# Performance work log

Hardware: AMD Instinct MI355X
Metric: run time of the kernel (lower is better)

Reference implementation:

```python
import jax, jax.numpy as jnp
import numpy as np
from jax import lax

B, T = 64, 256
N_INPUT, H, R, N_OUT, F = 161, 1024, 1024, 161, 64
KF, KT = 21, 11  # context
CONV_H = (N_INPUT - KF) // 2 + 1  # 71
RNN_IN = F * CONV_H  # 4544


def setup_inputs() -> dict:
    key = jax.random.key(0)
    ks = iter(jax.random.split(key, 40))
    s = 0.05
    rn = lambda shape, scale=s: jax.random.normal(next(ks), shape, jnp.float32) * scale
    inp = {
        'x': rn((B, 1, N_INPUT, T), 1.0),
        'h1': jnp.zeros((B, H), jnp.float32),
        'h2': jnp.zeros((B, H), jnp.float32),
        'h3': jnp.zeros((B, H), jnp.float32),
        # conv input layer
        'conv_W': rn((F, 1, KF, KT)),
        'conv_b': jnp.zeros((F,), jnp.float32),
        # GRU cells (bias=False), torch gate order [r, z, n]
        'W_ih0': rn((3 * H, RNN_IN)), 'W_hh0': rn((3 * H, H)),
        'W_ih1': rn((3 * H, H)),      'W_hh1': rn((3 * H, H)),
        'W_ih2': rn((3 * H, H)),      'W_hh2': rn((3 * H, H)),
        # in_transitions (n_input -> H)
        'in1_W': rn((H, N_INPUT)), 'in1_b': jnp.zeros((H,), jnp.float32),
        'in2_W': rn((H, N_INPUT)), 'in2_b': jnp.zeros((H,), jnp.float32),
        # h_transitions (H -> H)
        'ht0_W': rn((H, H)), 'ht0_b': jnp.zeros((H,), jnp.float32),
        'ht1_W': rn((H, H)), 'ht1_b': jnp.zeros((H,), jnp.float32),
        'ht2_W': rn((H, H)), 'ht2_b': jnp.zeros((H,), jnp.float32),
        # out_transitions (H -> R)
        'ot0_W': rn((R, H)), 'ot0_b': jnp.zeros((R,), jnp.float32),
        'ot1_W': rn((R, H)), 'ot1_b': jnp.zeros((R,), jnp.float32),
        'ot2_W': rn((R, H)), 'ot2_b': jnp.zeros((R,), jnp.float32),
        # output layer (R -> n_output), init uniform(-0.1, 0.1), bias 0
        'out_W': jax.random.uniform(next(ks), (N_OUT, R), jnp.float32, -0.1, 0.1),
        'out_b': jnp.zeros((N_OUT,), jnp.float32),
    }
    return inp


def _gru(x_gates, h, W_hh):
    # x_gates: (B, 3H) = x @ W_ih.T ; torch GRUCell, no bias
    hg = h @ W_hh.T
    xr, xz, xn = jnp.split(x_gates, 3, axis=-1)
    hr, hz, hn = jnp.split(hg, 3, axis=-1)
    r = jax.nn.sigmoid(xr + hr)
    z = jax.nn.sigmoid(xz + hz)
    n = jnp.tanh(xn + r * hn)
    return (1.0 - z) * n + z * h


def reference(x, h1, h2, h3, conv_W, conv_b,
              W_ih0, W_hh0, W_ih1, W_hh1, W_ih2, W_hh2,
              in1_W, in1_b, in2_W, in2_b,
              ht0_W, ht0_b, ht1_W, ht1_b, ht2_W, ht2_b,
              ot0_W, ot0_b, ot1_W, ot1_b, ot2_W, ot2_b,
              out_W, out_b):
    pad_t = (KT - 1) // 2
    # Conv2d(1, F, (21,11), stride=(2,1), padding=(0,5)) -> (B, F, CONV_H, T)
    y_conv = lax.conv_general_dilated(
        x, conv_W, window_strides=(2, 1), padding=((0, 0), (pad_t, pad_t)),
        dimension_numbers=('NCHW', 'OIHW', 'NCHW')) + conv_b[None, :, None, None]
    b, t = x.shape[0], x.shape[3]
    x_rnn = y_conv.reshape(b, RNN_IN, t).transpose(2, 0, 1)  # (T, B, RNN_IN)
    x0 = x[:, 0, :, :].transpose(2, 0, 1)                    # (T, B, N_INPUT)
    # Precompute all time-parallel input projections (big GEMMs outside scan)
    xg0 = jnp.einsum('tbi,gi->tbg', x_rnn, W_ih0)            # (T, B, 3H)
    x2_all = x0 @ in1_W.T + in1_b                            # (T, B, H)
    x3_all = x0 @ in2_W.T + in2_b                            # (T, B, H)

    def step(carry, inp):
        h1, h2, h3 = carry
        xg0_t, x2_t, x3_t = inp
        h1 = _gru(xg0_t, h1, W_hh0)
        h1_to_h2 = h1 @ ht0_W.T + ht0_b
        h1_to_h3 = h1 @ ht1_W.T + ht1_b
        r1 = h1 @ ot0_W.T + ot0_b
        h2 = _gru((x2_t + h1_to_h2) @ W_ih1.T, h2, W_hh1)
        h2_to_h3 = h1_to_h2 @ ht2_W.T + ht2_b  # note: applied to h1_to_h2, as in source
        r2 = h2 @ ot1_W.T + ot1_b
        h3 = _gru((x3_t + h1_to_h3 + h2_to_h3) @ W_ih2.T, h3, W_hh2)
        r3 = h3 @ ot2_W.T + ot2_b
        y_t = (r1 + r2 + r3) @ out_W.T + out_b
        return (h1, h2, h3), y_t

    _, y = lax.scan(step, (h1, h2, h3), (xg0, x2_all, x3_all))
    return y  # (T, B, N_OUT)
```

## Files before the change

### kernel.cpp

```cpp
#include <hip/hip_runtime.h>
#include <hip/hip_cooperative_groups.h>
#include <stdint.h>

namespace cg = cooperative_groups;

typedef __bf16 bf16x8 __attribute__((ext_vector_type(8)));
typedef float f32x4 __attribute__((ext_vector_type(4)));

#define MFMA16(a,b,c) __builtin_amdgcn_mfma_f32_16x16x32_bf16((a),(b),(c),0,0,0)

__device__ __forceinline__ float bf2f(unsigned short u){
  union { float f; unsigned int i; } v; v.i = ((unsigned int)u)<<16; return v.f;
}
__device__ __forceinline__ unsigned short f2bf(float f){
  union { float f; unsigned int i; } v; v.f = f;
  unsigned int r = v.i + 0x7FFFu + ((v.i>>16)&1u);
  return (unsigned short)(r>>16);
}
__device__ __forceinline__ bf16x8 ldg8(const unsigned short* p){ return *(const bf16x8*)p; }
__device__ __forceinline__ bf16x8 lds8(const short* p){ return *(const bf16x8*)p; }
__device__ __forceinline__ float sigm(float x){ return 1.f/(1.f+__expf(-x)); }
__device__ __forceinline__ float tanhc(float x){
  x = fminf(fmaxf(x,-30.f),30.f);
  float e = __expf(2.f*x);
  return (e-1.f)/(e+1.f);
}

__device__ __forceinline__ void wait_ge(unsigned int* c, int need){
  if (need <= 0) return;
  int guard = 0;
  while ((int)__hip_atomic_load(c, __ATOMIC_RELAXED, __HIP_MEMORY_SCOPE_AGENT) < need){
    __builtin_amdgcn_s_sleep(8);
    if (++guard > 4000000) break;
  }
}


__global__ void k_f2b(unsigned short* __restrict__ dst, const float* __restrict__ src, int n){
  int i = blockIdx.x*256 + threadIdx.x;
  if (i < n) dst[i] = f2bf(src[i]);
}

__global__ void k_zero(unsigned int* __restrict__ p, int nwords){
  int i = blockIdx.x*256 + threadIdx.x;
  if (i < nwords) p[i] = 0u;
}

__global__ void k_transpose(unsigned short* __restrict__ dst, const float* __restrict__ src,
                            int DR, int DC, int srcRowLen){
  __shared__ float tile[32][33];
  int r0 = blockIdx.x*32, c0 = blockIdx.y*32;
  int tx = threadIdx.x, ty = threadIdx.y;
  #pragma unroll
  for (int i=0;i<4;i++){
    int c = c0 + ty + i*8, r = r0 + tx;
    float v = 0.f;
    if (c < DC && r < srcRowLen) v = src[(size_t)c*srcRowLen + r];
    tile[ty+i*8][tx] = v;
  }
  __syncthreads();
  #pragma unroll
  for (int i=0;i<4;i++){
    int r = r0 + ty + i*8, c = c0 + tx;
    if (r < DR && c < DC) dst[(size_t)r*DC + c] = f2bf(tile[tx][ty+i*8]);
  }
}

__global__ void k_im2col(unsigned short* __restrict__ Xcol, const float* __restrict__ x, int t0){
  long long idx = (long long)blockIdx.x*256 + threadIdx.x;
  if (idx >= (long long)8192*1792) return;
  int row = (int)(idx / 1792), c = (int)(idx % 1792);
  int t = t0 + (row >> 6), b = row & 63;
  float v = 0.f;
  if (c < 1771){
    int kt = c / 161, i = c % 161;
    int tt = t + kt - 5;
    if (tt >= 0 && tt < 256) v = x[((size_t)b*161 + i)*256 + tt];
  }
  Xcol[idx] = f2bf(v);
}

__global__ void k_x0p(unsigned short* __restrict__ x0p, const float* __restrict__ x){
  int idx = blockIdx.x*256 + threadIdx.x;
  if (idx >= 16384*192) return;
  int row = idx / 192, i = idx % 192;
  int t = row >> 6, b = row & 63;
  float v = 0.f;
  if (i < 161) v = x[((size_t)b*161 + i)*256 + t];
  x0p[idx] = f2bf(v);
}

__global__ void k_cmatT(unsigned short* __restrict__ dst, const float* __restrict__ convW){
  int idx = blockIdx.x*256 + threadIdx.x;
  if (idx >= 1792*4544) return;
  int crow = idx / 4544, col = idx % 4544;
  float v = 0.f;
  if (crow < 1771){
    int kt = crow / 161, i = crow % 161;
    int f = col / 71, ch = col % 71;
    int kf = i - 2*ch;
    if (kf >= 0 && kf < 21) v = convW[((size_t)f*21 + kf)*11 + kt];
  }
  dst[idx] = f2bf(v);
}

__global__ void k_cbexp(float* __restrict__ dst, const float* __restrict__ convb){
  int i = blockIdx.x*256 + threadIdx.x;
  if (i < 4544) dst[i] = convb[i/71];
}

__global__ void k_add4(float* __restrict__ dst, const float* a, const float* b,
                       const float* c, const float* d, int n){
  int i = blockIdx.x*256 + threadIdx.x;
  if (i >= n) return;
  float v = a ? a[i] : 0.f;
  if (b) v += b[i];
  if (c) v += c[i];
  if (d) v += d[i];
  dst[i] = v;
}

__global__ void k_matvec(float* __restrict__ out, const float* __restrict__ A, int lda, int K,
                         const float* __restrict__ v, const float* __restrict__ addv, int M){
  int row = blockIdx.x*4 + (threadIdx.x>>6);
  int lane = threadIdx.x & 63;
  if (row >= M) return;
  float s = 0.f;
  for (int k = lane; k < K; k += 64) s += A[(size_t)row*lda + k]*v[k];
  #pragma unroll
  for (int o=32;o;o>>=1) s += __shfl_down(s, o);
  if (lane == 0) out[row] = s + (addv ? addv[row] : 0.f);
}


__global__ __launch_bounds__(256,1) void k_gemm_fast(
    unsigned short* __restrict__ C, const unsigned short* __restrict__ A,
    const unsigned short* __restrict__ B, const float* __restrict__ bias,
    int M, int N, int K, int lda, int ldb, int ldc)
{
  constexpr int LDT = 72;
  __shared__ unsigned short As[128*LDT];
  __shared__ unsigned short Bs[128*LDT];
  const int tid = threadIdx.x, wave = tid>>6, lane = tid&63;
  const int q = lane>>4, l15 = lane&15;
  const int m0 = blockIdx.x*128, n0 = blockIdx.y*128;
  const int mh = (wave>>1)*64, nh = (wave&1)*64;
  const int srow = tid>>3, scol = (tid&7)*8;
  f32x4 acc[4][4];
  #pragma unroll
  for (int i=0;i<4;i++)
    #pragma unroll
    for (int j=0;j<4;j++){ acc[i][j][0]=0.f; acc[i][j][1]=0.f; acc[i][j][2]=0.f; acc[i][j][3]=0.f; }

  for (int k0 = 0; k0 < K; k0 += 64){
    __syncthreads();
    #pragma unroll
    for (int p=0;p<4;p++){
      int r = p*32 + srow;
      *(bf16x8*)&As[r*LDT + scol] = ldg8(&A[(size_t)(m0+r)*lda + k0 + scol]);
      *(bf16x8*)&Bs[r*LDT + scol] = ldg8(&B[(size_t)(n0+r)*ldb + k0 + scol]);
    }
    __syncthreads();
    #pragma unroll
    for (int kc=0; kc<64; kc+=32){
      bf16x8 af[4], bf[4];
      #pragma unroll
      for (int i=0;i<4;i++) af[i] = *(const bf16x8*)&As[(mh + i*16 + l15)*LDT + kc + q*8];
      #pragma unroll
      for (int i=0;i<4;i++) bf[i] = *(const bf16x8*)&Bs[(nh + i*16 + l15)*LDT + kc + q*8];
      #pragma unroll
      for (int i=0;i<4;i++)
        #pragma unroll
        for (int j=0;j<4;j++)
          acc[i][j] = MFMA16(af[i], bf[j], acc[i][j]);
    }
  }
  #pragma unroll
  for (int i=0;i<4;i++){
    #pragma unroll
    for (int j=0;j<4;j++){
      int n = n0 + nh + j*16 + l15;
      float bz = bias ? bias[n] : 0.f;
      #pragma unroll
      for (int r=0;r<4;r++){
        int m = m0 + mh + i*16 + q*4 + r;
        C[(size_t)m*ldc + n] = f2bf(acc[i][j][r] + bz);
      }
    }
  }
}

__global__ __launch_bounds__(256,1) void k_gemm_small(
    unsigned short* __restrict__ C, const unsigned short* __restrict__ A,
    const unsigned short* __restrict__ B, const float* __restrict__ bias,
    const float* __restrict__ addT, int addT_ld,
    int M, int N, int K, int lda, int ldb, int ldc)
{
  constexpr int LDT = 40;
  __shared__ unsigned short As[64*LDT];
  __shared__ unsigned short Bs[64*LDT];
  const int tid = threadIdx.x, wave = tid>>6, lane = tid&63;
  const int q = lane>>4, l15 = lane&15;
  const int m0 = blockIdx.x*64, n0 = blockIdx.y*64;
  const int srow = tid>>2, scol = (tid&3)*8;
  f32x4 acc[4];
  #pragma unroll
  for (int j=0;j<4;j++){ acc[j][0]=0.f; acc[j][1]=0.f; acc[j][2]=0.f; acc[j][3]=0.f; }

  for (int k0=0;k0<K;k0+=32){
    __syncthreads();
    bf16x8 av;
    int gm = m0 + srow;
    if (gm < M) av = ldg8(&A[(size_t)gm*lda + k0 + scol]);
    else av = (bf16x8){(__bf16)0.f,(__bf16)0.f,(__bf16)0.f,(__bf16)0.f,(__bf16)0.f,(__bf16)0.f,(__bf16)0.f,(__bf16)0.f};
    bf16x8 bv = ldg8(&B[(size_t)(n0+srow)*ldb + k0 + scol]);
    *(bf16x8*)&As[srow*LDT + scol] = av;
    *(bf16x8*)&Bs[srow*LDT + scol] = bv;
    __syncthreads();
    bf16x8 af = *(const bf16x8*)&As[(wave*16 + l15)*LDT + q*8];
    #pragma unroll
    for (int j=0;j<4;j++){
      bf16x8 bf = *(const bf16x8*)&Bs[(j*16 + l15)*LDT + q*8];
      acc[j] = MFMA16(af, bf, acc[j]);
    }
  }
  #pragma unroll
  for (int j=0;j<4;j++){
    int n = n0 + j*16 + l15;
    float bz = bias ? bias[n] : 0.f;
    #pragma unroll
    for (int r=0;r<4;r++){
      int m = m0 + wave*16 + q*4 + r;
      if (m < M){
        float v = acc[j][r] + bz;
        if (addT) v += addT[(size_t)n*addT_ld + m];
        C[(size_t)m*ldc + n] = f2bf(v);
      }
    }
  }
}


struct ScanP {
  const unsigned short *W21, *W31, *Whh0, *Whh1, *Whh2, *Acat, *xg0, *x0p;
  const float *bc2, *bc3, *ybias;
  const float *h1in, *h2in, *h3in;
  float *h1f, *h2f, *h3f;
  unsigned short *hcat;
  unsigned int *cnt;
  float *out;
};

#define SCAN_BLOCKS 203
#define SCAN_LDS 145920

__global__ __launch_bounds__(256,1) void k_scan(ScanP p){
  extern __shared__ char smem[];
  short* lds = (short*)smem;
  const int bid = blockIdx.x, tid = threadIdx.x;
  const int wave = tid>>6, lane = tid&63;
  const int q = lane>>4, l15 = lane&15;
  unsigned int* c1 = p.cnt;
  unsigned int* c2 = p.cnt + 32;
  unsigned int* c3 = p.cnt + 64;
  unsigned int* cy = p.cnt + 96;

  for (int i = bid*256 + tid; i < 65536; i += SCAN_BLOCKS*256){
    int b = i>>10, j = i&1023;
    float v1 = p.h1in[i], v2 = p.h2in[i], v3 = p.h3in[i];
    p.h1f[65536+i]=v1; p.h2f[65536+i]=v2; p.h3f[65536+i]=v3;
    unsigned short* hc = p.hcat + 7*196608 + b*3072;
    hc[j]      = f2bf(v1);
    hc[1024+j] = f2bf(v2);
    hc[2048+j] = f2bf(v3);
  }

  if (bid < 64){
    int j0 = bid*16;
    for (int it = tid; it < 6144; it += 256){
      int row = it>>7, c8 = (it&127)*8;
      int grow = (row>>4)*1024 + j0 + (row&15);
      *(bf16x8*)&lds[row*1032 + c8] = ldg8(&p.Whh0[(size_t)grow*1024 + c8]);
    }
  } else if (bid < 192){
    int j0 = ((bid-64)&63)*16;
    const unsigned short* Wx = (bid<128) ? p.W21 : p.W31;
    const unsigned short* Wh = (bid<128) ? p.Whh1 : p.Whh2;
    for (int it = tid; it < 7296; it += 256){
      int row = it/152, c8 = (it%152)*8;
      int grow = (row>>4)*1024 + j0 + (row&15);
      *(bf16x8*)&lds[row*1224 + c8] = ldg8(&Wx[(size_t)grow*1216 + c8]);
    }
    for (int it = tid; it < 1728; it += 256){
      int row = it/36, c8 = (it%36)*8;
      int grow = (row>>4)*1024 + j0 + (row&15);
      *(bf16x8*)&lds[58752 + row*296 + c8] = ldg8(&Wh[(size_t)grow*1024 + c8]);
    }
  } else {
    int n0 = (bid-192)*16;
    for (int it = tid; it < 6144; it += 256){
      int row = it/384, c8 = (it%384)*8;
      *(bf16x8*)&lds[row*3080 + c8] = ldg8(&p.Acat[(size_t)(n0+row)*3072 + c8]);
    }
  }

  cg::grid_group grid = cg::this_grid();
  grid.sync();

  if (bid < 64){
    int j0 = bid*16;
    const short* b0 = lds + (0*16 + l15)*1032 + q*8;
    const short* b1 = lds + (1*16 + l15)*1032 + q*8;
    const short* b2 = lds + (2*16 + l15)*1032 + q*8;
    for (int t = 0; t < 256; ++t){
      if (tid == 0){
        wait_ge(c1, 64*t);
        wait_ge(c2, 64*(t-7));
        wait_ge(c3, 64*(t-7));
        wait_ge(cy, 11*(t-7));
        __threadfence();
      }
      __syncthreads();
      const unsigned short* h1b = p.hcat + (size_t)((t+7)&7)*196608;
      const unsigned short* ap = h1b + (size_t)(wave*16 + l15)*3072 + q*8;
      f32x4 a0,a1,a2;
      a0[0]=a0[1]=a0[2]=a0[3]=0.f; a1=a0; a2=a0;
      #pragma unroll 8
      for (int kc=0;kc<1024;kc+=32){
        bf16x8 av = ldg8(ap + kc);
        a0 = MFMA16(av, lds8(b0+kc), a0);
        a1 = MFMA16(av, lds8(b1+kc), a1);
        a2 = MFMA16(av, lds8(b2+kc), a2);
      }
      int jc = j0 + l15;
      const unsigned short* xg = p.xg0 + (size_t)t*196608;
      const float* hprev = p.h1f + ((t+1)&1)*65536;
      float* hnew = p.h1f + (t&1)*65536;
      unsigned short* hc = p.hcat + (size_t)(t&7)*196608;
      #pragma unroll
      for (int r=0;r<4;r++){
        int b = wave*16 + q*4 + r;
        float xr = bf2f(xg[b*3072 + jc]);
        float xz = bf2f(xg[b*3072 + 1024 + jc]);
        float xn = bf2f(xg[b*3072 + 2048 + jc]);
        float rg = sigm(xr + a0[r]);
        float zg = sigm(xz + a1[r]);
        float ng = tanhc(xn + rg*a2[r]);
        float hp = hprev[b*1024 + jc];
        float h = (1.f-zg)*ng + zg*hp;
        hnew[b*1024 + jc] = h;
        hc[b*3072 + jc] = f2bf(h);
      }
      __syncthreads();
      if (tid == 0){
        __threadfence();
        atomicAdd(c1, 1u);
      }
    }
  } else if (bid < 192){
    bool is2 = (bid < 128);
    int j0 = ((bid-64)&63)*16;
    const unsigned short* Wh = is2 ? p.Whh1 : p.Whh2;
    const float* bc = is2 ? p.bc2 : p.bc3;
    float* hf = is2 ? p.h2f : p.h3f;
    unsigned int* cown = is2 ? c2 : c3;
    int coff = is2 ? 1024 : 2048;
    const short* bx0 = lds + (0*16 + l15)*1224 + q*8;
    const short* bx1 = lds + (1*16 + l15)*1224 + q*8;
    const short* bx2 = lds + (2*16 + l15)*1224 + q*8;
    const short* bl0 = lds + 58752 + (0*16 + l15)*296 + q*8;
    const short* bl1 = lds + 58752 + (1*16 + l15)*296 + q*8;
    const short* bl2 = lds + 58752 + (2*16 + l15)*296 + q*8;
    const unsigned short* bg0 = Wh + (size_t)(0*1024 + j0 + l15)*1024 + q*8;
    const unsigned short* bg1 = Wh + (size_t)(1*1024 + j0 + l15)*1024 + q*8;
    const unsigned short* bg2 = Wh + (size_t)(2*1024 + j0 + l15)*1024 + q*8;
    for (int t = 0; t < 256; ++t){
      if (tid == 0){
        wait_ge(c1, 64*(t+1));
        wait_ge(cown, 64*t);
        wait_ge(cy, 11*(t-7));
        __threadfence();
      }
      __syncthreads();
      const unsigned short* slotT  = p.hcat + (size_t)(t&7)*196608;
      const unsigned short* slotT1 = p.hcat + (size_t)((t+7)&7)*196608;
      const unsigned short* a1p = slotT + (size_t)(wave*16 + l15)*3072 + q*8;
      const unsigned short* a2p = slotT1 + coff + (size_t)(wave*16 + l15)*3072 + q*8;
      f32x4 x0a,x1a,x2a,h0a,h1a,h2a;
      x0a[0]=x0a[1]=x0a[2]=x0a[3]=0.f; x1a=x0a; x2a=x0a; h0a=x0a; h1a=x0a; h2a=x0a;
      #pragma unroll 3
      for (int kc=0;kc<288;kc+=32){
        bf16x8 av = ldg8(a1p + kc);
        x0a = MFMA16(av, lds8(bx0+kc), x0a);
        x1a = MFMA16(av, lds8(bx1+kc), x1a);
        x2a = MFMA16(av, lds8(bx2+kc), x2a);
        bf16x8 ah = ldg8(a2p + kc);
        h0a = MFMA16(ah, lds8(bl0+kc), h0a);
        h1a = MFMA16(ah, lds8(bl1+kc), h1a);
        h2a = MFMA16(ah, lds8(bl2+kc), h2a);
      }
      #pragma unroll 4
      for (int kc=288;kc<1024;kc+=32){
        bf16x8 av = ldg8(a1p + kc);
        x0a = MFMA16(av, lds8(bx0+kc), x0a);
        x1a = MFMA16(av, lds8(bx1+kc), x1a);
        x2a = MFMA16(av, lds8(bx2+kc), x2a);
        bf16x8 ah = ldg8(a2p + kc);
        h0a = MFMA16(ah, ldg8(bg0+kc), h0a);
        h1a = MFMA16(ah, ldg8(bg1+kc), h1a);
        h2a = MFMA16(ah, ldg8(bg2+kc), h2a);
      }
      const unsigned short* xp = p.x0p + (size_t)(t*64 + wave*16 + l15)*192 + q*8;
      #pragma unroll
      for (int kc=0;kc<192;kc+=32){
        bf16x8 av = ldg8(xp + kc);
        x0a = MFMA16(av, lds8(bx0+1024+kc), x0a);
        x1a = MFMA16(av, lds8(bx1+1024+kc), x1a);
        x2a = MFMA16(av, lds8(bx2+1024+kc), x2a);
      }
      int jc = j0 + l15;
      float bcr = bc[jc], bcz = bc[1024+jc], bcn = bc[2048+jc];
      const float* hprev = hf + ((t+1)&1)*65536;
      float* hnw = hf + (t&1)*65536;
      unsigned short* hc = p.hcat + (size_t)(t&7)*196608 + coff;
      #pragma unroll
      for (int r=0;r<4;r++){
        int b = wave*16 + q*4 + r;
        float rg = sigm(x0a[r] + bcr + h0a[r]);
        float zg = sigm(x1a[r] + bcz + h1a[r]);
        float ng = tanhc(x2a[r] + bcn + rg*h2a[r]);
        float hp = hprev[b*1024 + jc];
        float h = (1.f-zg)*ng + zg*hp;
        hnw[b*1024 + jc] = h;
        hc[b*3072 + jc] = f2bf(h);
      }
      __syncthreads();
      if (tid == 0){
        __threadfence();
        atomicAdd(cown, 1u);
      }
    }
  } else {
    int n0 = (bid-192)*16;
    const short* bp = lds + l15*3080 + q*8;
    for (int t = 0; t < 256; ++t){
      if (tid == 0){
        wait_ge(c1, 64*(t+1));
        wait_ge(c2, 64*(t+1));
        wait_ge(c3, 64*(t+1));
        __threadfence();
      }
      __syncthreads();
      const unsigned short* hb = p.hcat + (size_t)(t&7)*196608;
      const unsigned short* ap = hb + (size_t)(wave*16 + l15)*3072 + q*8;
      f32x4 acc; acc[0]=acc[1]=acc[2]=acc[3]=0.f;
      #pragma unroll 8
      for (int kc=0;kc<3072;kc+=32){
        acc = MFMA16(ldg8(ap+kc), lds8(bp+kc), acc);
      }
      int o = n0 + l15;
      if (o < 161){
        float yb = p.ybias[o];
        #pragma unroll
        for (int r=0;r<4;r++){
          int b = wave*16 + q*4 + r;
          p.out[((size_t)t*64 + b)*161 + o] = acc[r] + yb;
        }
      }
      __syncthreads();
      if (tid == 0){
        __threadfence();
        atomicAdd(cy, 1u);
      }
    }
  }
}


extern "C" void kernel_launch(void* const* d_in, const int* in_sizes, int n_in,
                              void* d_out, int out_size, void* d_ws, size_t ws_size,
                              hipStream_t stream)
{
  const float* x      = (const float*)d_in[0];
  const float* h1in   = (const float*)d_in[1];
  const float* h2in   = (const float*)d_in[2];
  const float* h3in   = (const float*)d_in[3];
  const float* convW  = (const float*)d_in[4];
  const float* convb  = (const float*)d_in[5];
  const float* Wih0   = (const float*)d_in[6];
  const float* Whh0   = (const float*)d_in[7];
  const float* Wih1   = (const float*)d_in[8];
  const float* Whh1   = (const float*)d_in[9];
  const float* Wih2   = (const float*)d_in[10];
  const float* Whh2   = (const float*)d_in[11];
  const float* in1W   = (const float*)d_in[12];
  const float* in1b   = (const float*)d_in[13];
  const float* in2W   = (const float*)d_in[14];
  const float* in2b   = (const float*)d_in[15];
  const float* ht0W   = (const float*)d_in[16];
  const float* ht0b   = (const float*)d_in[17];
  const float* ht1W   = (const float*)d_in[18];
  const float* ht1b   = (const float*)d_in[19];
  const float* ht2W   = (const float*)d_in[20];
  const float* ht2b   = (const float*)d_in[21];
  const float* ot0W   = (const float*)d_in[22];
  const float* ot0b   = (const float*)d_in[23];
  const float* ot1W   = (const float*)d_in[24];
  const float* ot1b   = (const float*)d_in[25];
  const float* ot2W   = (const float*)d_in[26];
  const float* ot2b   = (const float*)d_in[27];
  const float* outW   = (const float*)d_in[28];
  const float* outb   = (const float*)d_in[29];
  (void)in_sizes; (void)n_in;

  char* base = (char*)d_ws;
  size_t off = 0;
  auto alloc = [&](size_t bytes)->void* {
    void* p = base + off;
    off += (bytes + 255) & ~(size_t)255;
    return p;
  };

  unsigned short* xg0   = (unsigned short*)alloc((size_t)16384*3072*2);
  unsigned short* x0p   = (unsigned short*)alloc((size_t)16384*192*2);
  unsigned short* W21   = (unsigned short*)alloc((size_t)3072*1216*2);
  unsigned short* W31   = (unsigned short*)alloc((size_t)3072*1216*2);
  unsigned short* Whh0b = (unsigned short*)alloc((size_t)3072*1024*2);
  unsigned short* Whh1b = (unsigned short*)alloc((size_t)3072*1024*2);
  unsigned short* Whh2b = (unsigned short*)alloc((size_t)3072*1024*2);
  unsigned short* Acat  = (unsigned short*)alloc((size_t)176*3072*2);
  unsigned short* hcat  = (unsigned short*)alloc((size_t)8*196608*2);
  float* h1f   = (float*)alloc((size_t)2*65536*4);
  float* h2f   = (float*)alloc((size_t)2*65536*4);
  float* h3f   = (float*)alloc((size_t)2*65536*4);
  unsigned int* cnt = (unsigned int*)alloc(512);
  float* bc2   = (float*)alloc(3072*4);
  float* bc3   = (float*)alloc(3072*4);
  float* bg1   = (float*)alloc(3072*4);
  float* ybias = (float*)alloc(161*4);
  float* cbexp = (float*)alloc(4544*4);
  float* vb2   = (float*)alloc(1024*4);
  float* t1    = (float*)alloc(1024*4);
  float* vb3   = (float*)alloc(1024*4);
  float* vbo   = (float*)alloc(1024*4);

  char* arena = (char*)alloc((size_t)3072*4544*2 + (size_t)1792*4544*2);
  unsigned short* Wih0b = (unsigned short*)arena;
  unsigned short* CmatT = (unsigned short*)(arena + (size_t)3072*4544*2);
  unsigned short* Weff  = (unsigned short*)W21;
  unsigned short* Xcol  = (unsigned short*)arena;
  char* a3 = arena;
  auto alloc3 = [&](size_t bytes)->void*{ void* p=a3; a3 += (bytes+255)&~(size_t)255; return p; };
  unsigned short* Wih1b = (unsigned short*)alloc3((size_t)3072*1024*2);
  unsigned short* Wih2b = (unsigned short*)alloc3((size_t)3072*1024*2);
  unsigned short* ht0T  = (unsigned short*)alloc3((size_t)1024*1024*2);
  unsigned short* ht2bf = (unsigned short*)alloc3((size_t)1024*1024*2);
  unsigned short* VT    = (unsigned short*)alloc3((size_t)1024*1024*2);
  unsigned short* in1T  = (unsigned short*)alloc3((size_t)192*1024*2);
  unsigned short* in2T  = (unsigned short*)alloc3((size_t)192*1024*2);
  unsigned short* ot0T  = (unsigned short*)alloc3((size_t)1024*1024*2);
  unsigned short* ot1T  = (unsigned short*)alloc3((size_t)1024*1024*2);
  unsigned short* ot2T  = (unsigned short*)alloc3((size_t)1024*1024*2);
  unsigned short* outWb = (unsigned short*)alloc3((size_t)161*1024*2);

  if (off > ws_size){
    hipMemsetAsync(d_out, 0, (size_t)out_size*sizeof(float), stream);
    return;
  }

  auto g1 = [](int n){ return dim3((n+255)/256); };
  dim3 tb(32,8);

  k_f2b<<<g1(3072*4544),256,0,stream>>>(Wih0b, Wih0, 3072*4544);
  k_cmatT<<<g1(1792*4544),256,0,stream>>>(CmatT, convW);
  k_gemm_fast<<<dim3(24,14),256,0,stream>>>(Weff, Wih0b, CmatT, nullptr,
                                            3072, 1792, 4544, 4544, 4544, 1792);

  k_cbexp<<<g1(4544),256,0,stream>>>(cbexp, convb);
  k_matvec<<<dim3(768),256,0,stream>>>(bg1, Wih0, 4544, 4544, cbexp, nullptr, 3072);
  k_im2col<<<dim3(57344),256,0,stream>>>(Xcol, x, 0);
  k_gemm_fast<<<dim3(64,24),256,0,stream>>>(xg0, Xcol, Weff, bg1,
                                            8192, 3072, 1792, 1792, 1792, 3072);
  k_im2col<<<dim3(57344),256,0,stream>>>(Xcol, x, 128);
  k_gemm_fast<<<dim3(64,24),256,0,stream>>>(xg0 + (size_t)8192*3072, Xcol, Weff, bg1,
                                            8192, 3072, 1792, 1792, 1792, 3072);

  k_f2b<<<g1(3072*1024),256,0,stream>>>(Wih1b, Wih1, 3072*1024);
  k_f2b<<<g1(3072*1024),256,0,stream>>>(Wih2b, Wih2, 3072*1024);
  k_f2b<<<g1(3072*1024),256,0,stream>>>(Whh0b, Whh0, 3072*1024);
  k_f2b<<<g1(3072*1024),256,0,stream>>>(Whh1b, Whh1, 3072*1024);
  k_f2b<<<g1(3072*1024),256,0,stream>>>(Whh2b, Whh2, 3072*1024);
  k_f2b<<<g1(1024*1024),256,0,stream>>>(ht2bf, ht2W, 1024*1024);
  k_f2b<<<g1(161*1024),256,0,stream>>>(outWb, outW, 161*1024);

  k_transpose<<<dim3(32,32),tb,0,stream>>>(ht0T, ht0W, 1024, 1024, 1024);
  k_transpose<<<dim3(6,32),tb,0,stream>>>(in1T, in1W, 192, 1024, 161);
  k_transpose<<<dim3(6,32),tb,0,stream>>>(in2T, in2W, 192, 1024, 161);
  k_transpose<<<dim3(32,32),tb,0,stream>>>(ot0T, ot0W, 1024, 1024, 1024);
  k_transpose<<<dim3(32,32),tb,0,stream>>>(ot1T, ot1W, 1024, 1024, 1024);
  k_transpose<<<dim3(32,32),tb,0,stream>>>(ot2T, ot2W, 1024, 1024, 1024);

  k_x0p<<<g1(16384*192),256,0,stream>>>(x0p, x);
  k_zero<<<g1(176*3072*2/4),256,0,stream>>>((unsigned int*)Acat, 176*3072*2/4);
  k_zero<<<dim3(1),256,0,stream>>>(cnt, 128);

  k_add4<<<g1(1024),256,0,stream>>>(vb2, in1b, ht0b, nullptr, nullptr, 1024);
  k_matvec<<<dim3(256),256,0,stream>>>(t1, ht2W, 1024, 1024, ht0b, nullptr, 1024);
  k_add4<<<g1(1024),256,0,stream>>>(vb3, in2b, ht1b, ht2b, t1, 1024);
  k_add4<<<g1(1024),256,0,stream>>>(vbo, ot0b, ot1b, ot2b, nullptr, 1024);
  k_matvec<<<dim3(768),256,0,stream>>>(bc2, Wih1, 1024, 1024, vb2, nullptr, 3072);
  k_matvec<<<dim3(768),256,0,stream>>>(bc3, Wih2, 1024, 1024, vb3, nullptr, 3072);
  k_matvec<<<dim3(41),256,0,stream>>>(ybias, outW, 1024, 1024, vbo, outb, 161);

  k_gemm_small<<<dim3(16,16),256,0,stream>>>(VT, ht0T, ht2bf, nullptr, ht1W, 1024,
                                             1024, 1024, 1024, 1024, 1024, 1024);
  k_gemm_small<<<dim3(48,16),256,0,stream>>>(W21, Wih1b, ht0T, nullptr, nullptr, 0,
                                             3072, 1024, 1024, 1024, 1024, 1216);
  k_gemm_small<<<dim3(48,3),256,0,stream>>>(W21+1024, Wih1b, in1T, nullptr, nullptr, 0,
                                             3072, 192, 1024, 1024, 1024, 1216);
  k_gemm_small<<<dim3(48,16),256,0,stream>>>(W31, Wih2b, VT, nullptr, nullptr, 0,
                                             3072, 1024, 1024, 1024, 1024, 1216);
  k_gemm_small<<<dim3(48,3),256,0,stream>>>(W31+1024, Wih2b, in2T, nullptr, nullptr, 0,
                                             3072, 192, 1024, 1024, 1024, 1216);
  k_gemm_small<<<dim3(3,16),256,0,stream>>>(Acat, outWb, ot0T, nullptr, nullptr, 0,
                                            161, 1024, 1024, 1024, 1024, 3072);
  k_gemm_small<<<dim3(3,16),256,0,stream>>>(Acat+1024, outWb, ot1T, nullptr, nullptr, 0,
                                            161, 1024, 1024, 1024, 1024, 3072);
  k_gemm_small<<<dim3(3,16),256,0,stream>>>(Acat+2048, outWb, ot2T, nullptr, nullptr, 0,
                                            161, 1024, 1024, 1024, 1024, 3072);

  hipFuncSetAttribute((const void*)k_scan, hipFuncAttributeMaxDynamicSharedMemorySize, SCAN_LDS);
  ScanP sp;
  sp.W21 = W21; sp.W31 = W31; sp.Whh0 = Whh0b; sp.Whh1 = Whh1b; sp.Whh2 = Whh2b;
  sp.Acat = Acat; sp.xg0 = xg0; sp.x0p = x0p;
  sp.bc2 = bc2; sp.bc3 = bc3; sp.ybias = ybias;
  sp.h1in = h1in; sp.h2in = h2in; sp.h3in = h3in;
  sp.h1f = h1f; sp.h2f = h2f; sp.h3f = h3f;
  sp.hcat = hcat; sp.cnt = cnt; sp.out = (float*)d_out;
  void* args[] = { &sp };
  hipLaunchCooperativeKernel((const void*)k_scan, dim3(SCAN_BLOCKS), dim3(256),
                             args, SCAN_LDS, stream);
}
```

Baseline: 8.798 ms.

## Repartition layer-2/3 GRU blocks to 12 columns so W_hh fits fully in LDS

Layers 2 and 3 of the persistent scan kernel now use 86 blocks each, every block owning 12 hidden columns instead of 16. This frees enough LDS to hold the whole W_hh slice, so the recurrent GEMM no longer streams most of W_hh from global memory on each timestep. The grid grows from 203 to 247 blocks and the counter thresholds are updated to match. In exchange, 4 of every 16 MFMA output lanes do wasted work, and the cooperative grid must still fit one block per CU.

```diff
diff --git a/kernel.cpp b/kernel.cpp
--- a/kernel.cpp
+++ b/kernel.cpp
@@ -251,8 +251,8 @@
   float *out;
 };
 
-#define SCAN_BLOCKS 203
-#define SCAN_LDS 145920
+#define SCAN_BLOCKS 247
+#define SCAN_LDS 162432
 
 __global__ __launch_bounds__(256,1) void k_scan(ScanP p){
   extern __shared__ char smem[];
@@ -282,22 +282,26 @@
       int grow = (row>>4)*1024 + j0 + (row&15);
       *(bf16x8*)&lds[row*1032 + c8] = ldg8(&p.Whh0[(size_t)grow*1024 + c8]);
     }
-  } else if (bid < 192){
-    int j0 = ((bid-64)&63)*16;
-    const unsigned short* Wx = (bid<128) ? p.W21 : p.W31;
-    const unsigned short* Wh = (bid<128) ? p.Whh1 : p.Whh2;
-    for (int it = tid; it < 7296; it += 256){
+  } else if (bid < 236){
+    bool is2 = (bid < 150);
+    int jb = is2 ? (bid-64) : (bid-150);
+    int j0 = jb*12;
+    const unsigned short* Wx = is2 ? p.W21 : p.W31;
+    const unsigned short* Wh = is2 ? p.Whh1 : p.Whh2;
+    for (int it = tid; it < 5472; it += 256){
       int row = it/152, c8 = (it%152)*8;
-      int grow = (row>>4)*1024 + j0 + (row&15);
-      *(bf16x8*)&lds[row*1224 + c8] = ldg8(&Wx[(size_t)grow*1216 + c8]);
-    }
-    for (int it = tid; it < 1728; it += 256){
-      int row = it/36, c8 = (it%36)*8;
-      int grow = (row>>4)*1024 + j0 + (row&15);
-      *(bf16x8*)&lds[58752 + row*296 + c8] = ldg8(&Wh[(size_t)grow*1024 + c8]);
+      int g = row/12, c = row - g*12;
+      int jj = j0 + c; if (jj > 1023) jj = 1023;
+      *(bf16x8*)&lds[row*1224 + c8] = ldg8(&Wx[(size_t)(g*1024 + jj)*1216 + c8]);
+    }
+    for (int it = tid; it < 4608; it += 256){
+      int row = it>>7, c8 = (it&127)*8;
+      int g = row/12, c = row - g*12;
+      int jj = j0 + c; if (jj > 1023) jj = 1023;
+      *(bf16x8*)&lds[44064 + row*1032 + c8] = ldg8(&Wh[(size_t)(g*1024 + jj)*1024 + c8]);
     }
   } else {
-    int n0 = (bid-192)*16;
+    int n0 = (bid-236)*16;
     for (int it = tid; it < 6144; it += 256){
       int row = it/384, c8 = (it%384)*8;
       *(bf16x8*)&lds[row*3080 + c8] = ldg8(&p.Acat[(size_t)(n0+row)*3072 + c8]);
@@ -315,8 +319,8 @@
     for (int t = 0; t < 256; ++t){
       if (tid == 0){
         wait_ge(c1, 64*t);
-        wait_ge(c2, 64*(t-7));
-        wait_ge(c3, 64*(t-7));
+        wait_ge(c2, 86*(t-7));
+        wait_ge(c3, 86*(t-7));
         wait_ge(cy, 11*(t-7));
         __threadfence();
       }
@@ -357,27 +361,28 @@
         atomicAdd(c1, 1u);
       }
     }
-  } else if (bid < 192){
-    bool is2 = (bid < 128);
-    int j0 = ((bid-64)&63)*16;
-    const unsigned short* Wh = is2 ? p.Whh1 : p.Whh2;
+  } else if (bid < 236){
+    bool is2 = (bid < 150);
+    int jb = is2 ? (bid-64) : (bid-150);
+    int j0 = jb*12;
     const float* bc = is2 ? p.bc2 : p.bc3;
     float* hf = is2 ? p.h2f : p.h3f;
     unsigned int* cown = is2 ? c2 : c3;
     int coff = is2 ? 1024 : 2048;
-    const short* bx0 = lds + (0*16 + l15)*1224 + q*8;
-    const short* bx1 = lds + (1*16 + l15)*1224 + q*8;
-    const short* bx2 = lds + (2*16 + l15)*1224 + q*8;
-    const short* bl0 = lds + 58752 + (0*16 + l15)*296 + q*8;
-    const short* bl1 = lds + 58752 + (1*16 + l15)*296 + q*8;
-    const short* bl2 = lds + 58752 + (2*16 + l15)*296 + q*8;
-    const unsigned short* bg0 = Wh + (size_t)(0*1024 + j0 + l15)*1024 + q*8;
-    const unsigned short* bg1 = Wh + (size_t)(1*1024 + j0 + l15)*1024 + q*8;
-    const unsigned short* bg2 = Wh + (size_t)(2*1024 + j0 + l15)*1024 + q*8;
+    int bl = (l15 < 12) ? l15 : 0;
+    const short* bx0 = lds + (0*12 + bl)*1224 + q*8;
+    const short* bx1 = lds + (1*12 + bl)*1224 + q*8;
+    const short* bx2 = lds + (2*12 + bl)*1224 + q*8;
+    const short* bh0 = lds + 44064 + (0*12 + bl)*1032 + q*8;
+    const short* bh1 = lds + 44064 + (1*12 + bl)*1032 + q*8;
+    const short* bh2 = lds + 44064 + (2*12 + bl)*1032 + q*8;
+    int jc = j0 + l15;
+    int jcc = (jc < 1024) ? jc : 1023;
+    bool valid = (l15 < 12) && (jc < 1024);
     for (int t = 0; t < 256; ++t){
       if (tid == 0){
         wait_ge(c1, 64*(t+1));
-        wait_ge(cown, 64*t);
+        wait_ge(cown, 86*t);
         wait_ge(cy, 11*(t-7));
         __threadfence();
       }
@@ -388,27 +393,16 @@
       const unsigned short* a2p = slotT1 + coff + (size_t)(wave*16 + l15)*3072 + q*8;
       f32x4 x0a,x1a,x2a,h0a,h1a,h2a;
       x0a[0]=x0a[1]=x0a[2]=x0a[3]=0.f; x1a=x0a; x2a=x0a; h0a=x0a; h1a=x0a; h2a=x0a;
-      #pragma unroll 3
-      for (int kc=0;kc<288;kc+=32){
+      #pragma unroll 4
+      for (int kc=0;kc<1024;kc+=32){
         bf16x8 av = ldg8(a1p + kc);
         x0a = MFMA16(av, lds8(bx0+kc), x0a);
         x1a = MFMA16(av, lds8(bx1+kc), x1a);
         x2a = MFMA16(av, lds8(bx2+kc), x2a);
         bf16x8 ah = ldg8(a2p + kc);
-        h0a = MFMA16(ah, lds8(bl0+kc), h0a);
-        h1a = MFMA16(ah, lds8(bl1+kc), h1a);
-        h2a = MFMA16(ah, lds8(bl2+kc), h2a);
-      }
-      #pragma unroll 4
-      for (int kc=288;kc<1024;kc+=32){
-        bf16x8 av = ldg8(a1p + kc);
-        x0a = MFMA16(av, lds8(bx0+kc), x0a);
-        x1a = MFMA16(av, lds8(bx1+kc), x1a);
-        x2a = MFMA16(av, lds8(bx2+kc), x2a);
-        bf16x8 ah = ldg8(a2p + kc);
-        h0a = MFMA16(ah, ldg8(bg0+kc), h0a);
-        h1a = MFMA16(ah, ldg8(bg1+kc), h1a);
-        h2a = MFMA16(ah, ldg8(bg2+kc), h2a);
+        h0a = MFMA16(ah, lds8(bh0+kc), h0a);
+        h1a = MFMA16(ah, lds8(bh1+kc), h1a);
+        h2a = MFMA16(ah, lds8(bh2+kc), h2a);
       }
       const unsigned short* xp = p.x0p + (size_t)(t*64 + wave*16 + l15)*192 + q*8;
       #pragma unroll
@@ -418,8 +412,7 @@
         x1a = MFMA16(av, lds8(bx1+1024+kc), x1a);
         x2a = MFMA16(av, lds8(bx2+1024+kc), x2a);
       }
-      int jc = j0 + l15;
-      float bcr = bc[jc], bcz = bc[1024+jc], bcn = bc[2048+jc];
+      float bcr = bc[jcc], bcz = bc[1024+jcc], bcn = bc[2048+jcc];
       const float* hprev = hf + ((t+1)&1)*65536;
       float* hnw = hf + (t&1)*65536;
       unsigned short* hc = p.hcat + (size_t)(t&7)*196608 + coff;
@@ -429,10 +422,12 @@
         float rg = sigm(x0a[r] + bcr + h0a[r]);
         float zg = sigm(x1a[r] + bcz + h1a[r]);
         float ng = tanhc(x2a[r] + bcn + rg*h2a[r]);
-        float hp = hprev[b*1024 + jc];
+        float hp = hprev[b*1024 + jcc];
         float h = (1.f-zg)*ng + zg*hp;
-        hnw[b*1024 + jc] = h;
-        hc[b*3072 + jc] = f2bf(h);
+        if (valid){
+          hnw[b*1024 + jc] = h;
+          hc[b*3072 + jc] = f2bf(h);
+        }
       }
       __syncthreads();
       if (tid == 0){
@@ -441,13 +436,13 @@
       }
     }
   } else {
-    int n0 = (bid-192)*16;
+    int n0 = (bid-236)*16;
     const short* bp = lds + l15*3080 + q*8;
     for (int t = 0; t < 256; ++t){
       if (tid == 0){
         wait_ge(c1, 64*(t+1));
-        wait_ge(c2, 64*(t+1));
-        wait_ge(c3, 64*(t+1));
+        wait_ge(c2, 86*(t+1));
+        wait_ge(c3, 86*(t+1));
         __threadfence();
       }
       __syncthreads();
```

After: 8.470 ms. -3.7%, faster.
